# Performance work log

Hardware: AMD Instinct MI355X
Metric: run time of the kernel (lower is better)

Reference implementation:

```python
import jax, jax.numpy as jnp
import numpy as np

N = 100000   # nodes
E = 1600000  # edges
S = 4        # state_dimension
H = 64       # hidden_channels


def _gcn_conv(x, row, col, W, b):
    """PyG GCNConv: h = x @ W; add self-loops; symmetric deg^-1/2 norm; scatter-add; + bias."""
    n = x.shape[0]
    h = x @ W  # [N, out]
    loop = jnp.arange(n, dtype=row.dtype)
    r = jnp.concatenate([row, loop])  # sources (with self-loops)
    c = jnp.concatenate([col, loop])  # targets (with self-loops)
    deg = jax.ops.segment_sum(jnp.ones(r.shape[0], h.dtype), c, num_segments=n)
    dinv = jnp.where(deg > 0, jax.lax.rsqrt(deg), 0.0)
    norm = dinv[r] * dinv[c]                      # [E+N]
    msg = h[r] * norm[:, None]                    # gather + scale, [E+N, out]
    out = jax.ops.segment_sum(msg, c, num_segments=n)  # scatter-add
    return out + b


def setup_inputs() -> dict:
    key = jax.random.key(0)
    k1, k2, k3, k4 = jax.random.split(key, 4)
    x = jax.random.normal(k1, (N, S), dtype=jnp.float32)
    edge_index = jax.random.randint(k2, (2, E), 0, N, dtype=jnp.int32)
    # Glorot-ish init for the two GCNConv linear layers (+ zero bias, PyG default)
    W1 = jax.random.normal(k3, (S, H), dtype=jnp.float32) * (1.0 / np.sqrt(S))
    b1 = jnp.zeros((H,), jnp.float32)
    W2 = jax.random.normal(k4, (H, S), dtype=jnp.float32) * (1.0 / np.sqrt(H))
    b2 = jnp.zeros((S,), jnp.float32)
    return {"x": x, "edge_index": edge_index, "W1": W1, "b1": b1, "W2": W2, "b2": b2}


def reference(x, edge_index, W1, b1, W2, b2):
    row, col = edge_index[0], edge_index[1]
    h = _gcn_conv(x, row, col, W1, b1)
    h = jax.nn.relu(h)
    out = _gcn_conv(h, row, col, W2, b2)
    return out
```

## Files before the change

### kernel.cpp

```cpp
#include <hip/hip_runtime.h>


#define CSHIFT 10
#define CNODES 1024
#define KC_MAX 128
#define CAPC   18432
#define EPB    4096
#define CURPAD 16
#define ANODES 256
#define ACAP   4864

__global__ void k_zero(int* __restrict__ p, int n) {
    int i = blockIdx.x * blockDim.x + threadIdx.x;
    if (i < n) p[i] = 0;
}

__global__ void __launch_bounds__(256) k_part(
        const int* __restrict__ row, const int* __restrict__ col,
        int e, int Kc, int* __restrict__ cursor, unsigned* __restrict__ ere) {
    __shared__ int h[KC_MAX];
    __shared__ int loff[KC_MAX];
    __shared__ int gbase[KC_MAX];
    __shared__ int lcur[KC_MAX];
    __shared__ unsigned staged[EPB];
    int t = threadIdx.x;
    if (t < KC_MAX) h[t] = 0;
    __syncthreads();
    int lo = blockIdx.x * EPB;
    int cbuf[16], rbuf[16];
#pragma unroll
    for (int k = 0; k < 16; ++k) {
        int i = lo + t + k * 256;
        if (i < e) { cbuf[k] = col[i]; rbuf[k] = row[i]; }
        else { cbuf[k] = -1; rbuf[k] = 0; }
    }
#pragma unroll
    for (int k = 0; k < 16; ++k)
        if (cbuf[k] >= 0) atomicAdd(&h[cbuf[k] >> CSHIFT], 1);
    __syncthreads();
    if (t < KC_MAX) loff[t] = h[t];
    __syncthreads();
    for (int off = 1; off < KC_MAX; off <<= 1) {
        int v = (t < KC_MAX && t >= off) ? loff[t - off] : 0;
        __syncthreads();
        if (t < KC_MAX) loff[t] += v;
        __syncthreads();
    }
    if (t < KC_MAX) {
        int st = loff[t] - h[t];
        loff[t] = st;
        lcur[t] = st;
        if (t < Kc && h[t]) gbase[t] = atomicAdd(&cursor[t * CURPAD], h[t]);
    }
    __syncthreads();
#pragma unroll
    for (int k = 0; k < 16; ++k) {
        int c = cbuf[k];
        if (c < 0) continue;
        int pos = atomicAdd(&lcur[c >> CSHIFT], 1);
        staged[pos] = ((unsigned)rbuf[k] << CSHIFT) | (unsigned)(c & (CNODES - 1));
    }
    __syncthreads();
    int wid = t >> 6, lane = t & 63;
    for (int k = wid; k < Kc; k += 4) {
        int len = h[k];
        if (!len) continue;
        int gb = gbase[k], lb = loff[k];
        size_t dst = (size_t)k * CAPC + gb;
        for (int j = lane; j < len; j += 64)
            if (gb + j < CAPC) ere[dst + j] = staged[lb + j];
    }
}

__global__ void __launch_bounds__(1024) k_sortN(
        const int* __restrict__ cursor, unsigned* __restrict__ ere,
        int* __restrict__ rstart, const float4* __restrict__ x,
        float* __restrict__ dinv, float4* __restrict__ y, int n) {
    __shared__ int hist[CNODES];
    __shared__ int lcur[CNODES];
    __shared__ unsigned sorted[CAPC];
    int b = blockIdx.x, t = threadIdx.x, nlo = b << CSHIFT;
    hist[t] = 0;
    __syncthreads();
    size_t c0 = (size_t)b * CAPC;
    int m = min(cursor[b * CURPAD], CAPC);
    int n4 = m >> 2;
    const uint4* e4 = (const uint4*)(ere + c0);
    for (int g = t; g < n4; g += 1024) {
        uint4 w = e4[g];
        atomicAdd(&hist[w.x & (CNODES - 1)], 1);
        atomicAdd(&hist[w.y & (CNODES - 1)], 1);
        atomicAdd(&hist[w.z & (CNODES - 1)], 1);
        atomicAdd(&hist[w.w & (CNODES - 1)], 1);
    }
    for (int i = (n4 << 2) + t; i < m; i += 1024)
        atomicAdd(&hist[ere[c0 + i] & (CNODES - 1)], 1);
    __syncthreads();
    int hv = hist[t];
    lcur[t] = hv;
    __syncthreads();
    for (int off = 1; off < CNODES; off <<= 1) {
        int v = (t >= off) ? lcur[t - off] : 0;
        __syncthreads();
        lcur[t] += v;
        __syncthreads();
    }
    int st = lcur[t] - hv;
    lcur[t] = st;
    rstart[(b << CSHIFT) + t] = (int)c0 + st;
    int node = nlo + t;
    if (node < n) {
        float di = rsqrtf((float)hv + 1.0f);
        dinv[node] = di;
        float4 xv = x[node];
        y[node] = make_float4(xv.x * di, xv.y * di, xv.z * di, xv.w * di);
    }
    __syncthreads();
    for (int g = t; g < n4; g += 1024) {
        uint4 w = e4[g];
        int p0 = atomicAdd(&lcur[w.x & (CNODES - 1)], 1); sorted[p0] = w.x >> CSHIFT;
        int p1 = atomicAdd(&lcur[w.y & (CNODES - 1)], 1); sorted[p1] = w.y >> CSHIFT;
        int p2 = atomicAdd(&lcur[w.z & (CNODES - 1)], 1); sorted[p2] = w.z >> CSHIFT;
        int p3 = atomicAdd(&lcur[w.w & (CNODES - 1)], 1); sorted[p3] = w.w >> CSHIFT;
    }
    for (int i = (n4 << 2) + t; i < m; i += 1024) {
        unsigned w = ere[c0 + i];
        int p = atomicAdd(&lcur[w & (CNODES - 1)], 1);
        sorted[p] = w >> CSHIFT;
    }
    __syncthreads();
    uint4* o4 = (uint4*)(ere + c0);
    for (int g = t; g < n4; g += 1024) o4[g] = ((uint4*)sorted)[g];
    for (int i = (n4 << 2) + t; i < m; i += 1024) ere[c0 + i] = sorted[i];
}

__global__ void __launch_bounds__(512) k_mid(
        const unsigned* __restrict__ ere, const int* __restrict__ rstart,
        const int* __restrict__ cursor, const float* __restrict__ dinv,
        const float4* __restrict__ x, const float4* __restrict__ y,
        const float* __restrict__ W1, const float* __restrict__ b1,
        const float* __restrict__ W2, const float* __restrict__ b2,
        float4* __restrict__ z, float4* __restrict__ out, int n) {
    __shared__ unsigned recs[ACAP];
    __shared__ float4 sums[ANODES];
    int g = blockIdx.x, t = threadIdx.x;
    int nlo = g * ANODES;
    int b = nlo >> CSHIFT;
    int s0 = rstart[nlo];
    int e0 = ((g & 3) == 3) ? (int)((size_t)b * CAPC) + min(cursor[b * CURPAD], CAPC)
                            : rstart[nlo + ANODES];
    int len = min(e0 - s0, ACAP);
    for (int i = t; i < len; i += 512) recs[i] = ere[s0 + i];
    __syncthreads();
    int tt = t >> 1, half = t & 1;
    int s = rstart[nlo + tt] - s0;
    int epos = ((tt == ANODES - 1) ? len : min(rstart[nlo + tt + 1] - s0, len));
    float vx = 0.f, vy = 0.f, vz = 0.f, vw = 0.f;
    int i = s + half;
    while (i + 6 < epos) {
        int r0 = recs[i], r1 = recs[i + 2], r2 = recs[i + 4], r3 = recs[i + 6];
        float4 a0 = y[r0], a1 = y[r1], a2 = y[r2], a3 = y[r3];
        vx += a0.x + a1.x + a2.x + a3.x;
        vy += a0.y + a1.y + a2.y + a3.y;
        vz += a0.z + a1.z + a2.z + a3.z;
        vw += a0.w + a1.w + a2.w + a3.w;
        i += 8;
    }
    for (; i < epos; i += 2) {
        float4 a = y[recs[i]];
        vx += a.x; vy += a.y; vz += a.z; vw += a.w;
    }
    vx += __shfl_xor(vx, 1);
    vy += __shfl_xor(vy, 1);
    vz += __shfl_xor(vz, 1);
    vw += __shfl_xor(vw, 1);
    if (half == 0) sums[tt] = make_float4(vx, vy, vz, vw);
    __syncthreads();
    int node = nlo + t;
    if (t < ANODES && node < n) {
        float di = dinv[node], sl = di * di;
        float4 sv = sums[t];
        float4 xv = x[node];
        float a0 = di * sv.x + xv.x * sl;
        float a1 = di * sv.y + xv.y * sl;
        float a2 = di * sv.z + xv.z * sl;
        float a3 = di * sv.w + xv.w * sl;
        float t0 = 0.f, t1 = 0.f, t2 = 0.f, t3 = 0.f;
#pragma unroll 8
        for (int j = 0; j < 64; ++j) {
            float h = b1[j] + a0 * W1[j] + a1 * W1[64 + j] + a2 * W1[128 + j] + a3 * W1[192 + j];
            h = fmaxf(h, 0.f);
            t0 += h * W2[j * 4 + 0];
            t1 += h * W2[j * 4 + 1];
            t2 += h * W2[j * 4 + 2];
            t3 += h * W2[j * 4 + 3];
        }
        z[node] = make_float4(t0 * di, t1 * di, t2 * di, t3 * di);
        out[node] = make_float4(b2[0] + t0 * sl, b2[1] + t1 * sl,
                                b2[2] + t2 * sl, b2[3] + t3 * sl);
    }
}

__global__ void __launch_bounds__(512) k_acc2(
        const unsigned* __restrict__ ere, const int* __restrict__ rstart,
        const int* __restrict__ cursor, const float* __restrict__ dinv,
        const float4* __restrict__ z, float4* __restrict__ out, int n) {
    __shared__ unsigned recs[ACAP];
    int g = blockIdx.x, t = threadIdx.x;
    int nlo = g * ANODES;
    int b = nlo >> CSHIFT;
    int s0 = rstart[nlo];
    int e0 = ((g & 3) == 3) ? (int)((size_t)b * CAPC) + min(cursor[b * CURPAD], CAPC)
                            : rstart[nlo + ANODES];
    int len = min(e0 - s0, ACAP);
    for (int i = t; i < len; i += 512) recs[i] = ere[s0 + i];
    __syncthreads();
    int tt = t >> 1, half = t & 1;
    int s = rstart[nlo + tt] - s0;
    int epos = ((tt == ANODES - 1) ? len : min(rstart[nlo + tt + 1] - s0, len));
    float vx = 0.f, vy = 0.f, vz = 0.f, vw = 0.f;
    int i = s + half;
    while (i + 6 < epos) {
        int r0 = recs[i], r1 = recs[i + 2], r2 = recs[i + 4], r3 = recs[i + 6];
        float4 a0 = z[r0], a1 = z[r1], a2 = z[r2], a3 = z[r3];
        vx += a0.x + a1.x + a2.x + a3.x;
        vy += a0.y + a1.y + a2.y + a3.y;
        vz += a0.z + a1.z + a2.z + a3.z;
        vw += a0.w + a1.w + a2.w + a3.w;
        i += 8;
    }
    for (; i < epos; i += 2) {
        float4 a = z[recs[i]];
        vx += a.x; vy += a.y; vz += a.z; vw += a.w;
    }
    vx += __shfl_xor(vx, 1);
    vy += __shfl_xor(vy, 1);
    vz += __shfl_xor(vz, 1);
    vw += __shfl_xor(vw, 1);
    int node = nlo + tt;
    if (half == 0 && node < n) {
        float di = dinv[node];
        float4 o = out[node];
        out[node] = make_float4(o.x + di * vx, o.y + di * vy,
                                o.z + di * vz, o.w + di * vw);
    }
}

extern "C" void kernel_launch(void* const* d_in, const int* in_sizes, int n_in,
                              void* d_out, int out_size, void* d_ws, size_t ws_size,
                              hipStream_t stream) {
    const float* x  = (const float*)d_in[0];
    const int* edge = (const int*)d_in[1];
    const float* W1 = (const float*)d_in[2];
    const float* b1 = (const float*)d_in[3];
    const float* W2 = (const float*)d_in[4];
    const float* b2 = (const float*)d_in[5];
    float* out = (float*)d_out;

    const int n = in_sizes[0] / 4;
    const int e = in_sizes[1] / 2;
    const int* row = edge;
    const int* col = edge + e;
    const int Kc = (n + CNODES - 1) >> CSHIFT;

    char* ws = (char*)d_ws;
    float* y    = (float*)ws;  ws += (size_t)4 * n * 4;
    float* zmid = (float*)ws;  ws += (size_t)4 * n * 4;
    float* dinv = (float*)ws;  ws += (size_t)n * 4;
    unsigned* ere = (unsigned*)ws;  ws += (size_t)Kc * CAPC * 4;
    int* cursor = (int*)ws;    ws += (size_t)Kc * CURPAD * 4;
    int* rstart = (int*)ws;    ws += (size_t)Kc * CNODES * 4;

    const int B = 256;
    const int gp = (e + EPB - 1) / EPB;
    const int ga = (n + ANODES - 1) / ANODES;
    const int nz = Kc * CURPAD;

    k_zero<<<(nz + B - 1) / B, B, 0, stream>>>(cursor, nz);
    k_part<<<gp, B, 0, stream>>>(row, col, e, Kc, cursor, ere);
    k_sortN<<<Kc, 1024, 0, stream>>>(cursor, ere, rstart, (const float4*)x,
                                     dinv, (float4*)y, n);
    k_mid<<<ga, 512, 0, stream>>>(ere, rstart, cursor, dinv, (const float4*)x,
                                  (const float4*)y, W1, b1, W2, b2,
                                  (float4*)zmid, (float4*)out, n);
    k_acc2<<<ga, 512, 0, stream>>>(ere, rstart, cursor, dinv,
                                   (const float4*)zmid, (float4*)out, n);
}
```

Baseline: 127.7 us.

## Split per-bucket sort across two blocks and halve aggregation block node count

The bucket sort now launches two blocks per 1024-node bucket, each sorting and writing back only the edges whose targets fall in its half. This doubles the number of sort blocks (about 98 to about 196) so more of the device's compute units are occupied, and shrinks shared memory per block. Both aggregation kernels now cover 128 nodes per block, with 4 threads per node instead of 2, and the partition kernel uses 512 threads with 8 edges each. In exchange, each sort block re-reads and histograms the whole bucket, duplicating that work, and there are more small aggregation blocks with extra shuffle reductions.

```diff
diff --git a/kernel.cpp b/kernel.cpp
--- a/kernel.cpp
+++ b/kernel.cpp
@@ -7,15 +7,16 @@
 #define CAPC   18432
 #define EPB    4096
 #define CURPAD 16
-#define ANODES 256
-#define ACAP   4864
+#define HCAP   9216
+#define ANODES 128
+#define ACAP   2432
 
 __global__ void k_zero(int* __restrict__ p, int n) {
     int i = blockIdx.x * blockDim.x + threadIdx.x;
     if (i < n) p[i] = 0;
 }
 
-__global__ void __launch_bounds__(256) k_part(
+__global__ void __launch_bounds__(512) k_part(
         const int* __restrict__ row, const int* __restrict__ col,
         int e, int Kc, int* __restrict__ cursor, unsigned* __restrict__ ere) {
     __shared__ int h[KC_MAX];
@@ -27,15 +28,15 @@
     if (t < KC_MAX) h[t] = 0;
     __syncthreads();
     int lo = blockIdx.x * EPB;
-    int cbuf[16], rbuf[16];
+    int cbuf[8], rbuf[8];
 #pragma unroll
-    for (int k = 0; k < 16; ++k) {
-        int i = lo + t + k * 256;
+    for (int k = 0; k < 8; ++k) {
+        int i = lo + t + k * 512;
         if (i < e) { cbuf[k] = col[i]; rbuf[k] = row[i]; }
         else { cbuf[k] = -1; rbuf[k] = 0; }
     }
 #pragma unroll
-    for (int k = 0; k < 16; ++k)
+    for (int k = 0; k < 8; ++k)
         if (cbuf[k] >= 0) atomicAdd(&h[cbuf[k] >> CSHIFT], 1);
     __syncthreads();
     if (t < KC_MAX) loff[t] = h[t];
@@ -54,7 +55,7 @@
     }
     __syncthreads();
 #pragma unroll
-    for (int k = 0; k < 16; ++k) {
+    for (int k = 0; k < 8; ++k) {
         int c = cbuf[k];
         if (c < 0) continue;
         int pos = atomicAdd(&lcur[c >> CSHIFT], 1);
@@ -62,7 +63,7 @@
     }
     __syncthreads();
     int wid = t >> 6, lane = t & 63;
-    for (int k = wid; k < Kc; k += 4) {
+    for (int k = wid; k < Kc; k += 8) {
         int len = h[k];
         if (!len) continue;
         int gb = gbase[k], lb = loff[k];
@@ -72,14 +73,15 @@
     }
 }
 
-__global__ void __launch_bounds__(1024) k_sortN(
+__global__ void __launch_bounds__(1024) k_sortH(
         const int* __restrict__ cursor, unsigned* __restrict__ ere,
         int* __restrict__ rstart, const float4* __restrict__ x,
         float* __restrict__ dinv, float4* __restrict__ y, int n) {
     __shared__ int hist[CNODES];
-    __shared__ int lcur[CNODES];
-    __shared__ unsigned sorted[CAPC];
-    int b = blockIdx.x, t = threadIdx.x, nlo = b << CSHIFT;
+    __shared__ int scn[CNODES];
+    __shared__ unsigned sorted[HCAP];
+    int b = blockIdx.x >> 1, half = blockIdx.x & 1;
+    int t = threadIdx.x, nlo = b << CSHIFT;
     hist[t] = 0;
     __syncthreads();
     size_t c0 = (size_t)b * CAPC;
@@ -97,41 +99,50 @@
         atomicAdd(&hist[ere[c0 + i] & (CNODES - 1)], 1);
     __syncthreads();
     int hv = hist[t];
-    lcur[t] = hv;
+    scn[t] = hv;
     __syncthreads();
     for (int off = 1; off < CNODES; off <<= 1) {
-        int v = (t >= off) ? lcur[t - off] : 0;
+        int v = (t >= off) ? scn[t - off] : 0;
         __syncthreads();
-        lcur[t] += v;
+        scn[t] += v;
         __syncthreads();
     }
-    int st = lcur[t] - hv;
-    lcur[t] = st;
+    int st = scn[t] - hv;
+    int hb1 = scn[511];
     rstart[(b << CSHIFT) + t] = (int)c0 + st;
-    int node = nlo + t;
-    if (node < n) {
-        float di = rsqrtf((float)hv + 1.0f);
-        dinv[node] = di;
-        float4 xv = x[node];
-        y[node] = make_float4(xv.x * di, xv.y * di, xv.z * di, xv.w * di);
-    }
+    if ((t >> 9) == half) {
+        int node = nlo + t;
+        if (node < n) {
+            float di = rsqrtf((float)hv + 1.0f);
+            dinv[node] = di;
+            float4 xv = x[node];
+            y[node] = make_float4(xv.x * di, xv.y * di, xv.z * di, xv.w * di);
+        }
+    }
+    int base = half ? hb1 : 0;
+    int cnt = half ? (m - hb1) : hb1;
+    __syncthreads();
+    scn[t] = st - base;
     __syncthreads();
     for (int g = t; g < n4; g += 1024) {
         uint4 w = e4[g];
-        int p0 = atomicAdd(&lcur[w.x & (CNODES - 1)], 1); sorted[p0] = w.x >> CSHIFT;
-        int p1 = atomicAdd(&lcur[w.y & (CNODES - 1)], 1); sorted[p1] = w.y >> CSHIFT;
-        int p2 = atomicAdd(&lcur[w.z & (CNODES - 1)], 1); sorted[p2] = w.z >> CSHIFT;
-        int p3 = atomicAdd(&lcur[w.w & (CNODES - 1)], 1); sorted[p3] = w.w >> CSHIFT;
+        int l0 = w.x & (CNODES - 1);
+        if ((l0 >> 9) == half) { int p = atomicAdd(&scn[l0], 1); if (p < HCAP) sorted[p] = w.x >> CSHIFT; }
+        int l1 = w.y & (CNODES - 1);
+        if ((l1 >> 9) == half) { int p = atomicAdd(&scn[l1], 1); if (p < HCAP) sorted[p] = w.y >> CSHIFT; }
+        int l2 = w.z & (CNODES - 1);
+        if ((l2 >> 9) == half) { int p = atomicAdd(&scn[l2], 1); if (p < HCAP) sorted[p] = w.z >> CSHIFT; }
+        int l3 = w.w & (CNODES - 1);
+        if ((l3 >> 9) == half) { int p = atomicAdd(&scn[l3], 1); if (p < HCAP) sorted[p] = w.w >> CSHIFT; }
     }
     for (int i = (n4 << 2) + t; i < m; i += 1024) {
         unsigned w = ere[c0 + i];
-        int p = atomicAdd(&lcur[w & (CNODES - 1)], 1);
-        sorted[p] = w >> CSHIFT;
-    }
-    __syncthreads();
-    uint4* o4 = (uint4*)(ere + c0);
-    for (int g = t; g < n4; g += 1024) o4[g] = ((uint4*)sorted)[g];
-    for (int i = (n4 << 2) + t; i < m; i += 1024) ere[c0 + i] = sorted[i];
+        int ln = w & (CNODES - 1);
+        if ((ln >> 9) == half) { int p = atomicAdd(&scn[ln], 1); if (p < HCAP) sorted[p] = w >> CSHIFT; }
+    }
+    __syncthreads();
+    int wb = min(cnt, HCAP);
+    for (int i = t; i < wb; i += 1024) ere[c0 + base + i] = sorted[i];
 }
 
 __global__ void __launch_bounds__(512) k_mid(
@@ -146,35 +157,36 @@
     int g = blockIdx.x, t = threadIdx.x;
     int nlo = g * ANODES;
     int b = nlo >> CSHIFT;
+    int c0i = (int)((size_t)b * CAPC);
     int s0 = rstart[nlo];
-    int e0 = ((g & 3) == 3) ? (int)((size_t)b * CAPC) + min(cursor[b * CURPAD], CAPC)
+    int e0 = ((g & 7) == 7) ? c0i + min(cursor[b * CURPAD], CAPC)
                             : rstart[nlo + ANODES];
     int len = min(e0 - s0, ACAP);
     for (int i = t; i < len; i += 512) recs[i] = ere[s0 + i];
     __syncthreads();
-    int tt = t >> 1, half = t & 1;
+    int tt = t >> 2, q = t & 3;
     int s = rstart[nlo + tt] - s0;
-    int epos = ((tt == ANODES - 1) ? len : min(rstart[nlo + tt + 1] - s0, len));
+    int epos = (tt == ANODES - 1) ? len : min(rstart[nlo + tt + 1] - s0, len);
     float vx = 0.f, vy = 0.f, vz = 0.f, vw = 0.f;
-    int i = s + half;
-    while (i + 6 < epos) {
-        int r0 = recs[i], r1 = recs[i + 2], r2 = recs[i + 4], r3 = recs[i + 6];
+    int i = s + q;
+    while (i + 12 < epos) {
+        int r0 = recs[i], r1 = recs[i + 4], r2 = recs[i + 8], r3 = recs[i + 12];
         float4 a0 = y[r0], a1 = y[r1], a2 = y[r2], a3 = y[r3];
         vx += a0.x + a1.x + a2.x + a3.x;
         vy += a0.y + a1.y + a2.y + a3.y;
         vz += a0.z + a1.z + a2.z + a3.z;
         vw += a0.w + a1.w + a2.w + a3.w;
-        i += 8;
-    }
-    for (; i < epos; i += 2) {
+        i += 16;
+    }
+    for (; i < epos; i += 4) {
         float4 a = y[recs[i]];
         vx += a.x; vy += a.y; vz += a.z; vw += a.w;
     }
-    vx += __shfl_xor(vx, 1);
-    vy += __shfl_xor(vy, 1);
-    vz += __shfl_xor(vz, 1);
-    vw += __shfl_xor(vw, 1);
-    if (half == 0) sums[tt] = make_float4(vx, vy, vz, vw);
+    vx += __shfl_xor(vx, 1); vx += __shfl_xor(vx, 2);
+    vy += __shfl_xor(vy, 1); vy += __shfl_xor(vy, 2);
+    vz += __shfl_xor(vz, 1); vz += __shfl_xor(vz, 2);
+    vw += __shfl_xor(vw, 1); vw += __shfl_xor(vw, 2);
+    if (q == 0) sums[tt] = make_float4(vx, vy, vz, vw);
     __syncthreads();
     int node = nlo + t;
     if (t < ANODES && node < n) {
@@ -206,43 +218,48 @@
         const int* __restrict__ cursor, const float* __restrict__ dinv,
         const float4* __restrict__ z, float4* __restrict__ out, int n) {
     __shared__ unsigned recs[ACAP];
+    __shared__ float4 sums[ANODES];
     int g = blockIdx.x, t = threadIdx.x;
     int nlo = g * ANODES;
     int b = nlo >> CSHIFT;
+    int c0i = (int)((size_t)b * CAPC);
     int s0 = rstart[nlo];
-    int e0 = ((g & 3) == 3) ? (int)((size_t)b * CAPC) + min(cursor[b * CURPAD], CAPC)
+    int e0 = ((g & 7) == 7) ? c0i + min(cursor[b * CURPAD], CAPC)
                             : rstart[nlo + ANODES];
     int len = min(e0 - s0, ACAP);
     for (int i = t; i < len; i += 512) recs[i] = ere[s0 + i];
     __syncthreads();
-    int tt = t >> 1, half = t & 1;
+    int tt = t >> 2, q = t & 3;
     int s = rstart[nlo + tt] - s0;
-    int epos = ((tt == ANODES - 1) ? len : min(rstart[nlo + tt + 1] - s0, len));
+    int epos = (tt == ANODES - 1) ? len : min(rstart[nlo + tt + 1] - s0, len);
     float vx = 0.f, vy = 0.f, vz = 0.f, vw = 0.f;
-    int i = s + half;
-    while (i + 6 < epos) {
-        int r0 = recs[i], r1 = recs[i + 2], r2 = recs[i + 4], r3 = recs[i + 6];
+    int i = s + q;
+    while (i + 12 < epos) {
+        int r0 = recs[i], r1 = recs[i + 4], r2 = recs[i + 8], r3 = recs[i + 12];
         float4 a0 = z[r0], a1 = z[r1], a2 = z[r2], a3 = z[r3];
         vx += a0.x + a1.x + a2.x + a3.x;
         vy += a0.y + a1.y + a2.y + a3.y;
         vz += a0.z + a1.z + a2.z + a3.z;
         vw += a0.w + a1.w + a2.w + a3.w;
-        i += 8;
-    }
-    for (; i < epos; i += 2) {
+        i += 16;
+    }
+    for (; i < epos; i += 4) {
         float4 a = z[recs[i]];
         vx += a.x; vy += a.y; vz += a.z; vw += a.w;
     }
-    vx += __shfl_xor(vx, 1);
-    vy += __shfl_xor(vy, 1);
-    vz += __shfl_xor(vz, 1);
-    vw += __shfl_xor(vw, 1);
-    int node = nlo + tt;
-    if (half == 0 && node < n) {
+    vx += __shfl_xor(vx, 1); vx += __shfl_xor(vx, 2);
+    vy += __shfl_xor(vy, 1); vy += __shfl_xor(vy, 2);
+    vz += __shfl_xor(vz, 1); vz += __shfl_xor(vz, 2);
+    vw += __shfl_xor(vw, 1); vw += __shfl_xor(vw, 2);
+    if (q == 0) sums[tt] = make_float4(vx, vy, vz, vw);
+    __syncthreads();
+    int node = nlo + t;
+    if (t < ANODES && node < n) {
         float di = dinv[node];
+        float4 sv = sums[t];
         float4 o = out[node];
-        out[node] = make_float4(o.x + di * vx, o.y + di * vy,
-                                o.z + di * vz, o.w + di * vw);
+        out[node] = make_float4(o.x + di * sv.x, o.y + di * sv.y,
+                                o.z + di * sv.z, o.w + di * sv.w);
     }
 }
 
@@ -277,9 +294,9 @@
     const int nz = Kc * CURPAD;
 
     k_zero<<<(nz + B - 1) / B, B, 0, stream>>>(cursor, nz);
-    k_part<<<gp, B, 0, stream>>>(row, col, e, Kc, cursor, ere);
-    k_sortN<<<Kc, 1024, 0, stream>>>(cursor, ere, rstart, (const float4*)x,
-                                     dinv, (float4*)y, n);
+    k_part<<<gp, 512, 0, stream>>>(row, col, e, Kc, cursor, ere);
+    k_sortH<<<2 * Kc, 1024, 0, stream>>>(cursor, ere, rstart, (const float4*)x,
+                                         dinv, (float4*)y, n);
     k_mid<<<ga, 512, 0, stream>>>(ere, rstart, cursor, dinv, (const float4*)x,
                                   (const float4*)y, W1, b1, W2, b2,
                                   (float4*)zmid, (float4*)out, n);
```

Result: no change. 125.9 us (-1.5%).
